# Kernel optimization log

Hardware: AMD Instinct MI355X
Metric: run time of the kernel (lower is better)

The kernel has to match this reference:

```python
import jax, jax.numpy as jnp
import numpy as np

N = 50000
E = 800000
D_IN, D_HID, D_OUT = 128, 128, 64


def _glorot(key, shape):
    fan_in, fan_out = shape[1], shape[0]
    lim = np.sqrt(6.0 / (fan_in + fan_out))
    return jax.random.uniform(key, shape, jnp.float32, -lim, lim)


def setup_inputs() -> dict:
    key = jax.random.key(0)
    ks = jax.random.split(key, 12)
    x = jax.random.normal(ks[0], (N, D_IN), jnp.float32)
    edge_index = jax.random.randint(ks[1], (2, E), 0, N, jnp.int32)
    edge_attr = jax.random.uniform(ks[2], (E,), jnp.float32)
    return {
        "x": x,
        "edge_index": edge_index,
        "edge_attr": edge_attr,
        # conv1: in -> hidden
        "W1_rel": _glorot(ks[3], (D_HID, D_IN)),
        "b1_rel": jnp.zeros((D_HID,), jnp.float32),
        "W1_root": _glorot(ks[4], (D_HID, D_IN)),
        # conv_mu: hidden -> out
        "Wmu_rel": _glorot(ks[5], (D_OUT, D_HID)),
        "bmu_rel": jnp.zeros((D_OUT,), jnp.float32),
        "Wmu_root": _glorot(ks[6], (D_OUT, D_HID)),
        # conv_logvar: hidden -> out
        "Wlv_rel": _glorot(ks[7], (D_OUT, D_HID)),
        "blv_rel": jnp.zeros((D_OUT,), jnp.float32),
        "Wlv_root": _glorot(ks[8], (D_OUT, D_HID)),
    }


def sage_conv(x, src, dst, ew, W_rel, b_rel, W_root, n_nodes):
    # message: edge_weight * x_j  (gather from source nodes)
    msg = x[src] * ew[:, None]                                   # [E, d]
    agg = jax.ops.segment_sum(msg, dst, num_segments=n_nodes)    # [N, d]
    cnt = jax.ops.segment_sum(jnp.ones_like(ew), dst, num_segments=n_nodes)
    mean = agg / jnp.maximum(cnt, 1.0)[:, None]                  # scatter-mean
    return mean @ W_rel.T + b_rel + x @ W_root.T


def reference(x, edge_index, edge_attr, W1_rel, b1_rel, W1_root,
              Wmu_rel, bmu_rel, Wmu_root, Wlv_rel, blv_rel, Wlv_root):
    src, dst = edge_index[0], edge_index[1]
    h = jax.nn.elu(sage_conv(x, src, dst, edge_attr, W1_rel, b1_rel, W1_root, N))
    mu = sage_conv(h, src, dst, edge_attr, Wmu_rel, bmu_rel, Wmu_root, N)
    logvar = sage_conv(h, src, dst, edge_attr, Wlv_rel, blv_rel, Wlv_root, N)
    return mu, logvar
```

## Files before the change

### kernel.cpp

```cpp
#include <hip/hip_runtime.h>
#include <hip/hip_bf16.h>
#include <math.h>

#define NNODES 50000
#define NEDGES 800000
#define NRANGE 6250
#define NC     64
#define CHUNK_E (NEDGES / NC)
#define NSLICE 4
#define SLICE_E (CHUNK_E / NSLICE)

using short8 = __attribute__((ext_vector_type(8))) short;
using f32x4  = __attribute__((ext_vector_type(4))) float;
typedef unsigned long long u64;

__device__ __forceinline__ short f2bf(float f) {
    __hip_bfloat16 h = __float2bfloat16(f);
    return *reinterpret_cast<short*>(&h);
}


__global__ __launch_bounds__(256)
void prep_kernel(const float* __restrict__ x, __hip_bfloat16* __restrict__ xb,
                 const float* __restrict__ w0, const float* __restrict__ w1,
                 const float* __restrict__ w2, const float* __restrict__ w3,
                 const float* __restrict__ w4, const float* __restrict__ w5,
                 __hip_bfloat16* __restrict__ Wb) {
    int b = blockIdx.x;
    int tid = threadIdx.x;
    if (b < 3125) {
        int i = b * 256 + tid;
        const float4* p = (const float4*)x + (size_t)i * 2;
        float4 a = p[0], c = p[1];
        short8 o;
        o[0] = f2bf(a.x); o[1] = f2bf(a.y); o[2] = f2bf(a.z); o[3] = f2bf(a.w);
        o[4] = f2bf(c.x); o[5] = f2bf(c.y); o[6] = f2bf(c.z); o[7] = f2bf(c.w);
        *reinterpret_cast<short8*>((short*)xb + (size_t)i * 8) = o;
    } else {
        int i = (b - 3125) * 256 + tid;
        const float* src; int off;
        if      (i < 16384) { src = w0; off = 0; }
        else if (i < 32768) { src = w1; off = 16384; }
        else if (i < 40960) { src = w2; off = 32768; }
        else if (i < 49152) { src = w3; off = 40960; }
        else if (i < 57344) { src = w4; off = 49152; }
        else                { src = w5; off = 57344; }
        Wb[i] = __float2bfloat16(src[i - off]);
    }
}


__global__ __launch_bounds__(256)
void hist_kernel(const int* __restrict__ dst, unsigned int* __restrict__ partial,
                 unsigned char* __restrict__ rank8) {
    __shared__ unsigned int hist[NNODES / 4];
    int c = blockIdx.x;
    int tid = threadIdx.x;
    for (int i = tid; i < NNODES / 4; i += 256) hist[i] = 0;
    __syncthreads();
    int base = c * CHUNK_E;
    for (int e = base + tid; e < base + CHUNK_E; e += 256) {
        int d = dst[e];
        int sh = 8 * (d & 3);
        unsigned int old = atomicAdd(&hist[d >> 2], 1u << sh);
        rank8[e] = (unsigned char)((old >> sh) & 0xffu);
    }
    __syncthreads();
    unsigned int* outp = partial + (size_t)c * (NNODES / 4);
    for (int i = tid; i < NNODES / 4; i += 256) outp[i] = hist[i];
}


__global__ __launch_bounds__(1024)
void scan1_kernel(const unsigned int* __restrict__ partial,
                  unsigned char* __restrict__ cbase,
                  int* __restrict__ excl, int* __restrict__ bsum) {
    __shared__ int sdata[1024];
    int tid = threadIdx.x;
    int n = blockIdx.x * 1024 + tid;
    int deg = 0;
    if (n < NNODES) {
        int sh = 8 * (n & 3);
        int idx = n >> 2;
        unsigned int packed = 0;
        unsigned int* cbout = (unsigned int*)(cbase + (size_t)n * NC);
#pragma unroll 4
        for (int c = 0; c < NC; ++c) {
            unsigned int w = partial[(size_t)c * (NNODES / 4) + idx];
            unsigned int cc = (w >> sh) & 0xffu;
            packed |= ((unsigned int)(deg & 0xff)) << (8 * (c & 3));
            deg += (int)cc;
            if ((c & 3) == 3) { cbout[c >> 2] = packed; packed = 0; }
        }
    }
    sdata[tid] = deg;
    __syncthreads();
    for (int off = 1; off < 1024; off <<= 1) {
        int t = (tid >= off) ? sdata[tid - off] : 0;
        __syncthreads();
        sdata[tid] += t;
        __syncthreads();
    }
    if (n < NNODES) excl[n] = sdata[tid] - deg;
    if (tid == 1023) bsum[blockIdx.x] = sdata[1023];
}

__global__ __launch_bounds__(64)
void scan2_kernel(int* __restrict__ bsum, int nb) {
    int lane = threadIdx.x;
    int v = (lane < nb) ? bsum[lane] : 0;
    int incl = v;
    for (int off = 1; off < 64; off <<= 1) {
        int t = __shfl_up(incl, off);
        if (lane >= off) incl += t;
    }
    if (lane < nb) bsum[lane] = incl - v;
    if (lane == 63) bsum[nb] = incl;
}


__global__ __launch_bounds__(256)
void fill_kernel(const int* __restrict__ src, const int* __restrict__ dst,
                 const float* __restrict__ ew,
                 const int* __restrict__ excl, const int* __restrict__ bsum,
                 const unsigned char* __restrict__ cbase,
                 const unsigned char* __restrict__ rank8,
                 u64* __restrict__ edges) {
    int b = blockIdx.x;
    int r = b & 7;
    int t = b >> 3;
    int c = t & (NC - 1);
    int s = t >> 6;
    int lo = r * NRANGE;
    int base = c * CHUNK_E + s * SLICE_E;
    int end = base + SLICE_E;
    for (int e = base + threadIdx.x; e < end; e += 256) {
        int d = dst[e];
        unsigned int dl = (unsigned int)(d - lo);
        if (dl < NRANGE) {
            int slot = excl[d] + bsum[d >> 10] + (int)cbase[(size_t)d * NC + c] + (int)rank8[e];
            u64 pack = ((u64)(unsigned int)__float_as_int(ew[e]) << 32) | (unsigned int)src[e];
            edges[slot] = pack;
        }
    }
}


__device__ __forceinline__ void gstep(u64 e, const unsigned int* __restrict__ Fb,
                                      int lane, float& ax, float& ay) {
    unsigned int v = Fb[(size_t)(unsigned int)e * 64 + lane];
    float w = __uint_as_float((unsigned int)(e >> 32));
    ax += __uint_as_float(v << 16) * w;
    ay += __uint_as_float(v & 0xffff0000u) * w;
}

__global__ __launch_bounds__(256)
void gather_mean_kernel(const unsigned int* __restrict__ Fb,
                        const int* __restrict__ excl, const int* __restrict__ bsum,
                        const u64* __restrict__ edges,
                        unsigned int* __restrict__ outb,
                        int n_nodes, int E) {
    int node = (blockIdx.x * blockDim.x + threadIdx.x) >> 6;
    int lane = threadIdx.x & 63;
    if (node >= n_nodes) return;
    int beg = excl[node] + bsum[node >> 10];
    int end = (node + 1 < n_nodes) ? (excl[node + 1] + bsum[(node + 1) >> 10]) : E;
    beg = __builtin_amdgcn_readfirstlane(beg);
    end = __builtin_amdgcn_readfirstlane(end);

    float ax[8], ay[8];
#pragma unroll
    for (int j = 0; j < 8; ++j) { ax[j] = 0.f; ay[j] = 0.f; }

    int s = beg;
    for (; s + 8 <= end; s += 8) {
        u64 e[8];
#pragma unroll
        for (int j = 0; j < 8; ++j) e[j] = __builtin_nontemporal_load(edges + s + j);
#pragma unroll
        for (int j = 0; j < 8; ++j) gstep(e[j], Fb, lane, ax[j], ay[j]);
    }
    if (s + 4 <= end) {
        u64 e[4];
#pragma unroll
        for (int j = 0; j < 4; ++j) e[j] = __builtin_nontemporal_load(edges + s + j);
#pragma unroll
        for (int j = 0; j < 4; ++j) gstep(e[j], Fb, lane, ax[j], ay[j]);
        s += 4;
    }
    if (s + 2 <= end) {
        u64 e0 = __builtin_nontemporal_load(edges + s);
        u64 e1 = __builtin_nontemporal_load(edges + s + 1);
        gstep(e0, Fb, lane, ax[0], ay[0]);
        gstep(e1, Fb, lane, ax[1], ay[1]);
        s += 2;
    }
    if (s < end) {
        u64 e0 = __builtin_nontemporal_load(edges + s);
        gstep(e0, Fb, lane, ax[0], ay[0]);
    }
#pragma unroll
    for (int j = 4; j < 8; ++j) { ax[j - 4] += ax[j]; ay[j - 4] += ay[j]; }
    float axs = (ax[0] + ax[1]) + (ax[2] + ax[3]);
    float ays = (ay[0] + ay[1]) + (ay[2] + ay[3]);
    float inv = 1.f / fmaxf((float)(end - beg), 1.f);
    unsigned int lo = (unsigned int)(unsigned short)f2bf(axs * inv);
    unsigned int hi = (unsigned int)(unsigned short)f2bf(ays * inv);
    outb[(size_t)node * 64 + lane] = lo | (hi << 16);
}


__global__ __launch_bounds__(256)
void linear1_mfma(const __hip_bfloat16* __restrict__ Ab1,
                  const __hip_bfloat16* __restrict__ Ab2,
                  const __hip_bfloat16* __restrict__ Wb,
                  const float* __restrict__ bias,
                  __hip_bfloat16* __restrict__ outb,
                  int n_nodes) {
    int wid  = threadIdx.x >> 6;
    int lane = threadIdx.x & 63;
    int nodeBase = blockIdx.x * 64 + wid * 16;
    int m  = lane & 15;
    int kq = lane >> 4;
    int node = nodeBase + m;
    int nodeC = (node < n_nodes) ? node : (n_nodes - 1);

    short8 a1[4], a2[4];
    const short* A1p = (const short*)Ab1 + (size_t)nodeC * 128 + kq * 8;
    const short* A2p = (const short*)Ab2 + (size_t)nodeC * 128 + kq * 8;
#pragma unroll
    for (int kk = 0; kk < 4; ++kk) {
        a1[kk] = *(const short8*)(A1p + kk * 32);
        a2[kk] = *(const short8*)(A2p + kk * 32);
    }
    const short* Wrel  = (const short*)Wb;
    const short* Wroot = (const short*)Wb + 16384;

#pragma unroll
    for (int c = 0; c < 8; ++c) {
        f32x4 acc = {0.f, 0.f, 0.f, 0.f};
        const short* b1p = Wrel  + (size_t)(c * 16 + m) * 128 + kq * 8;
        const short* b2p = Wroot + (size_t)(c * 16 + m) * 128 + kq * 8;
#pragma unroll
        for (int kk = 0; kk < 4; ++kk) {
            short8 bw1 = *(const short8*)(b1p + kk * 32);
            acc = __builtin_amdgcn_mfma_f32_16x16x32_bf16(a1[kk], bw1, acc, 0, 0, 0);
            short8 bw2 = *(const short8*)(b2p + kk * 32);
            acc = __builtin_amdgcn_mfma_f32_16x16x32_bf16(a2[kk], bw2, acc, 0, 0, 0);
        }
        int col = c * 16 + m;
        float b = bias[col];
#pragma unroll
        for (int i = 0; i < 4; ++i) {
            int gn = nodeBase + kq * 4 + i;
            if (gn < n_nodes) {
                float v = acc[i] + b;
                v = (v > 0.f) ? v : expm1f(v);
                outb[(size_t)gn * 128 + col] = __float2bfloat16(v);
            }
        }
    }
}

__global__ __launch_bounds__(256)
void linear2_mfma(const __hip_bfloat16* __restrict__ Ab1,
                  const __hip_bfloat16* __restrict__ Ab2,
                  const __hip_bfloat16* __restrict__ Wb,
                  const float* __restrict__ bmu, const float* __restrict__ blv,
                  float* __restrict__ out,
                  int n_nodes) {
    int wid  = threadIdx.x >> 6;
    int lane = threadIdx.x & 63;
    int nodeBase = blockIdx.x * 64 + wid * 16;
    int m  = lane & 15;
    int kq = lane >> 4;
    int node = nodeBase + m;
    int nodeC = (node < n_nodes) ? node : (n_nodes - 1);

    short8 a1[4], a2[4];
    const short* A1p = (const short*)Ab1 + (size_t)nodeC * 128 + kq * 8;
    const short* A2p = (const short*)Ab2 + (size_t)nodeC * 128 + kq * 8;
#pragma unroll
    for (int kk = 0; kk < 4; ++kk) {
        a1[kk] = *(const short8*)(A1p + kk * 32);
        a2[kk] = *(const short8*)(A2p + kk * 32);
    }
    const short* WmuR = (const short*)Wb + 32768;
    const short* WmuT = (const short*)Wb + 40960;
    const short* WlvR = (const short*)Wb + 49152;
    const short* WlvT = (const short*)Wb + 57344;

#pragma unroll
    for (int c = 0; c < 4; ++c) {
        f32x4 accMu = {0.f, 0.f, 0.f, 0.f};
        f32x4 accLv = {0.f, 0.f, 0.f, 0.f};
        size_t wrow = (size_t)(c * 16 + m) * 128 + kq * 8;
#pragma unroll
        for (int kk = 0; kk < 4; ++kk) {
            short8 bm1 = *(const short8*)(WmuR + wrow + kk * 32);
            accMu = __builtin_amdgcn_mfma_f32_16x16x32_bf16(a1[kk], bm1, accMu, 0, 0, 0);
            short8 bm2 = *(const short8*)(WmuT + wrow + kk * 32);
            accMu = __builtin_amdgcn_mfma_f32_16x16x32_bf16(a2[kk], bm2, accMu, 0, 0, 0);
            short8 bl1 = *(const short8*)(WlvR + wrow + kk * 32);
            accLv = __builtin_amdgcn_mfma_f32_16x16x32_bf16(a1[kk], bl1, accLv, 0, 0, 0);
            short8 bl2 = *(const short8*)(WlvT + wrow + kk * 32);
            accLv = __builtin_amdgcn_mfma_f32_16x16x32_bf16(a2[kk], bl2, accLv, 0, 0, 0);
        }
        int col = c * 16 + m;
        float bm = bmu[col], bl = blv[col];
#pragma unroll
        for (int i = 0; i < 4; ++i) {
            int gn = nodeBase + kq * 4 + i;
            if (gn < n_nodes) {
                out[(size_t)gn * 64 + col] = accMu[i] + bm;
                out[(size_t)NNODES * 64 + (size_t)gn * 64 + col] = accLv[i] + bl;
            }
        }
    }
}

extern "C" void kernel_launch(void* const* d_in, const int* in_sizes, int n_in,
                              void* d_out, int out_size, void* d_ws, size_t ws_size,
                              hipStream_t stream) {
    const float* x        = (const float*)d_in[0];
    const int*   eidx     = (const int*)d_in[1];
    const float* eattr    = (const float*)d_in[2];
    const float* W1_rel   = (const float*)d_in[3];
    const float* b1_rel   = (const float*)d_in[4];
    const float* W1_root  = (const float*)d_in[5];
    const float* Wmu_rel  = (const float*)d_in[6];
    const float* bmu_rel  = (const float*)d_in[7];
    const float* Wmu_root = (const float*)d_in[8];
    const float* Wlv_rel  = (const float*)d_in[9];
    const float* blv_rel  = (const float*)d_in[10];
    const float* Wlv_root = (const float*)d_in[11];
    float* out = (float*)d_out;

    const int N = NNODES, E = NEDGES;
    const int nb = (N + 1023) / 1024;
    const int* src = eidx;
    const int* dst = eidx + E;

    char* ws = (char*)d_ws;
    size_t off = 0;
    int* excl = (int*)(ws + off); off += (size_t)N * 4;
    int* bsum = (int*)(ws + off); off += 256;
    off = (off + 63) & ~(size_t)63;
    unsigned int* partial = (unsigned int*)(ws + off); off += (size_t)NC * (N / 4) * 4;
    unsigned char* cbase  = (unsigned char*)(ws + off); off += (size_t)N * NC;
    unsigned char* rank8  = (unsigned char*)(ws + off); off += (size_t)E;
    off = (off + 63) & ~(size_t)63;
    u64* edges = (u64*)(ws + off); off += (size_t)E * 8;
    __hip_bfloat16* xb    = (__hip_bfloat16*)(ws + off); off += (size_t)N * 128 * 2;
    __hip_bfloat16* meanb = (__hip_bfloat16*)(ws + off); off += (size_t)N * 128 * 2;
    __hip_bfloat16* hb    = (__hip_bfloat16*)(ws + off); off += (size_t)N * 128 * 2;
    __hip_bfloat16* Wb    = (__hip_bfloat16*)(ws + off); off += 65536 * 2;

    prep_kernel<<<3381, 256, 0, stream>>>(x, xb, W1_rel, W1_root, Wmu_rel, Wmu_root,
                                          Wlv_rel, Wlv_root, Wb);
    hist_kernel<<<NC, 256, 0, stream>>>(dst, partial, rank8);
    scan1_kernel<<<nb, 1024, 0, stream>>>(partial, cbase, excl, bsum);
    scan2_kernel<<<1, 64, 0, stream>>>(bsum, nb);
    fill_kernel<<<NC * 8 * NSLICE, 256, 0, stream>>>(src, dst, eattr, excl, bsum,
                                                     cbase, rank8, edges);

    gather_mean_kernel<<<(N * 64 + 255) / 256, 256, 0, stream>>>(
        (const unsigned int*)xb, excl, bsum, edges, (unsigned int*)meanb, N, E);
    linear1_mfma<<<(N + 63) / 64, 256, 0, stream>>>(meanb, xb, Wb, b1_rel, hb, N);
    gather_mean_kernel<<<(N * 64 + 255) / 256, 256, 0, stream>>>(
        (const unsigned int*)hb, excl, bsum, edges, (unsigned int*)meanb, N, E);
    linear2_mfma<<<(N + 63) / 64, 256, 0, stream>>>(meanb, hb, Wb, bmu_rel, blv_rel, out, N);
}
```

Measured before the change: 213.4 us.

## Slice feature matrices into column blocks for cache-local gathers; fuse histogram into prep

Stores the bf16 node features (x, mean, h) as four column slices of 32 features each, so each slice of the whole table (about 3.2 MB) is more likely to stay in cache during the random gather. The gather kernel now uses 16 lanes per node per slice, and blocks are interleaved across slice and node half so concurrent blocks hit the same slice. The linear kernels read and write through the sliced layout. The histogram kernel is merged into the prep launch to drop one launch. In exchange, the edge list is read four times per layer, and each 16-lane group has its own loop bound, so nodes with different degrees make those groups diverge within a wavefront.

```diff
diff --git a/kernel.cpp b/kernel.cpp
--- a/kernel.cpp
+++ b/kernel.cpp
@@ -9,6 +9,10 @@
 #define CHUNK_E (NEDGES / NC)
 #define NSLICE 4
 #define SLICE_E (CHUNK_E / NSLICE)
+#define NHALF (NNODES / 2)
+
+#define SLICE_STRIDE_U (NNODES * 16)
+#define SLICE_STRIDE_S (NNODES * 32)
 
 using short8 = __attribute__((ext_vector_type(8))) short;
 using f32x4  = __attribute__((ext_vector_type(4))) float;
@@ -25,19 +29,38 @@
                  const float* __restrict__ w0, const float* __restrict__ w1,
                  const float* __restrict__ w2, const float* __restrict__ w3,
                  const float* __restrict__ w4, const float* __restrict__ w5,
-                 __hip_bfloat16* __restrict__ Wb) {
+                 __hip_bfloat16* __restrict__ Wb,
+                 const int* __restrict__ dst, unsigned int* __restrict__ partial,
+                 unsigned char* __restrict__ rank8) {
+    __shared__ unsigned int hist[NNODES / 4];
     int b = blockIdx.x;
     int tid = threadIdx.x;
-    if (b < 3125) {
-        int i = b * 256 + tid;
-        const float4* p = (const float4*)x + (size_t)i * 2;
-        float4 a = p[0], c = p[1];
+    if (b < 64) {
+        int c = b;
+        for (int i = tid; i < NNODES / 4; i += 256) hist[i] = 0;
+        __syncthreads();
+        int base = c * CHUNK_E;
+        for (int e = base + tid; e < base + CHUNK_E; e += 256) {
+            int d = dst[e];
+            int sh = 8 * (d & 3);
+            unsigned int old = atomicAdd(&hist[d >> 2], 1u << sh);
+            rank8[e] = (unsigned char)((old >> sh) & 0xffu);
+        }
+        __syncthreads();
+        unsigned int* outp = partial + (size_t)c * (NNODES / 4);
+        for (int i = tid; i < NNODES / 4; i += 256) outp[i] = hist[i];
+    } else if (b < 3189) {
+        int i = (b - 64) * 256 + tid;
+        int node = i >> 4, t = i & 15;
+        const float4* p = (const float4*)(x + (size_t)node * 128 + t * 8);
+        float4 a = p[0], c4 = p[1];
         short8 o;
         o[0] = f2bf(a.x); o[1] = f2bf(a.y); o[2] = f2bf(a.z); o[3] = f2bf(a.w);
-        o[4] = f2bf(c.x); o[5] = f2bf(c.y); o[6] = f2bf(c.z); o[7] = f2bf(c.w);
-        *reinterpret_cast<short8*>((short*)xb + (size_t)i * 8) = o;
+        o[4] = f2bf(c4.x); o[5] = f2bf(c4.y); o[6] = f2bf(c4.z); o[7] = f2bf(c4.w);
+        short* dstp = (short*)xb + (size_t)(t >> 2) * SLICE_STRIDE_S + (size_t)node * 32 + (t & 3) * 8;
+        *reinterpret_cast<short8*>(dstp) = o;
     } else {
-        int i = (b - 3125) * 256 + tid;
+        int i = (b - 3189) * 256 + tid;
         const float* src; int off;
         if      (i < 16384) { src = w0; off = 0; }
         else if (i < 32768) { src = w1; off = 16384; }
@@ -47,27 +70,6 @@
         else                { src = w5; off = 57344; }
         Wb[i] = __float2bfloat16(src[i - off]);
     }
-}
-
-
-__global__ __launch_bounds__(256)
-void hist_kernel(const int* __restrict__ dst, unsigned int* __restrict__ partial,
-                 unsigned char* __restrict__ rank8) {
-    __shared__ unsigned int hist[NNODES / 4];
-    int c = blockIdx.x;
-    int tid = threadIdx.x;
-    for (int i = tid; i < NNODES / 4; i += 256) hist[i] = 0;
-    __syncthreads();
-    int base = c * CHUNK_E;
-    for (int e = base + tid; e < base + CHUNK_E; e += 256) {
-        int d = dst[e];
-        int sh = 8 * (d & 3);
-        unsigned int old = atomicAdd(&hist[d >> 2], 1u << sh);
-        rank8[e] = (unsigned char)((old >> sh) & 0xffu);
-    }
-    __syncthreads();
-    unsigned int* outp = partial + (size_t)c * (NNODES / 4);
-    for (int i = tid; i < NNODES / 4; i += 256) outp[i] = hist[i];
 }
 
 
@@ -146,9 +148,9 @@
 }
 
 
-__device__ __forceinline__ void gstep(u64 e, const unsigned int* __restrict__ Fb,
-                                      int lane, float& ax, float& ay) {
-    unsigned int v = Fb[(size_t)(unsigned int)e * 64 + lane];
+__device__ __forceinline__ void gstep16(u64 e, const unsigned int* __restrict__ F,
+                                        float& ax, float& ay) {
+    unsigned int v = F[(size_t)(unsigned int)e * 16];
     float w = __uint_as_float((unsigned int)(e >> 32));
     ax += __uint_as_float(v << 16) * w;
     ay += __uint_as_float(v & 0xffff0000u) * w;
@@ -159,54 +161,44 @@
                         const int* __restrict__ excl, const int* __restrict__ bsum,
                         const u64* __restrict__ edges,
                         unsigned int* __restrict__ outb,
-                        int n_nodes, int E) {
-    int node = (blockIdx.x * blockDim.x + threadIdx.x) >> 6;
-    int lane = threadIdx.x & 63;
-    if (node >= n_nodes) return;
+                        int E) {
+    int b = blockIdx.x;
+    int r = b & 7;
+    int slice = r & 3;
+    int half = r >> 2;
+    int nb = b >> 3;
+    int g = threadIdx.x >> 4;
+    int lane16 = threadIdx.x & 15;
+    int nlocal = nb * 16 + g;
+    if (nlocal >= NHALF) return;
+    int node = half * NHALF + nlocal;
     int beg = excl[node] + bsum[node >> 10];
-    int end = (node + 1 < n_nodes) ? (excl[node + 1] + bsum[(node + 1) >> 10]) : E;
-    beg = __builtin_amdgcn_readfirstlane(beg);
-    end = __builtin_amdgcn_readfirstlane(end);
-
-    float ax[8], ay[8];
-#pragma unroll
-    for (int j = 0; j < 8; ++j) { ax[j] = 0.f; ay[j] = 0.f; }
-
+    int end = (node + 1 < NNODES) ? (excl[node + 1] + bsum[(node + 1) >> 10]) : E;
+    const unsigned int* F = Fb + (size_t)slice * SLICE_STRIDE_U + lane16;
+
+    float ax0 = 0.f, ay0 = 0.f, ax1 = 0.f, ay1 = 0.f;
+    float ax2 = 0.f, ay2 = 0.f, ax3 = 0.f, ay3 = 0.f;
     int s = beg;
-    for (; s + 8 <= end; s += 8) {
-        u64 e[8];
-#pragma unroll
-        for (int j = 0; j < 8; ++j) e[j] = __builtin_nontemporal_load(edges + s + j);
-#pragma unroll
-        for (int j = 0; j < 8; ++j) gstep(e[j], Fb, lane, ax[j], ay[j]);
-    }
-    if (s + 4 <= end) {
-        u64 e[4];
-#pragma unroll
-        for (int j = 0; j < 4; ++j) e[j] = __builtin_nontemporal_load(edges + s + j);
-#pragma unroll
-        for (int j = 0; j < 4; ++j) gstep(e[j], Fb, lane, ax[j], ay[j]);
-        s += 4;
-    }
-    if (s + 2 <= end) {
+    for (; s + 4 <= end; s += 4) {
+        u64 e0 = __builtin_nontemporal_load(edges + s + 0);
+        u64 e1 = __builtin_nontemporal_load(edges + s + 1);
+        u64 e2 = __builtin_nontemporal_load(edges + s + 2);
+        u64 e3 = __builtin_nontemporal_load(edges + s + 3);
+        gstep16(e0, F, ax0, ay0);
+        gstep16(e1, F, ax1, ay1);
+        gstep16(e2, F, ax2, ay2);
+        gstep16(e3, F, ax3, ay3);
+    }
+    for (; s < end; ++s) {
         u64 e0 = __builtin_nontemporal_load(edges + s);
-        u64 e1 = __builtin_nontemporal_load(edges + s + 1);
-        gstep(e0, Fb, lane, ax[0], ay[0]);
-        gstep(e1, Fb, lane, ax[1], ay[1]);
-        s += 2;
-    }
-    if (s < end) {
-        u64 e0 = __builtin_nontemporal_load(edges + s);
-        gstep(e0, Fb, lane, ax[0], ay[0]);
-    }
-#pragma unroll
-    for (int j = 4; j < 8; ++j) { ax[j - 4] += ax[j]; ay[j - 4] += ay[j]; }
-    float axs = (ax[0] + ax[1]) + (ax[2] + ax[3]);
-    float ays = (ay[0] + ay[1]) + (ay[2] + ay[3]);
+        gstep16(e0, F, ax0, ay0);
+    }
+    float axs = (ax0 + ax1) + (ax2 + ax3);
+    float ays = (ay0 + ay1) + (ay2 + ay3);
     float inv = 1.f / fmaxf((float)(end - beg), 1.f);
     unsigned int lo = (unsigned int)(unsigned short)f2bf(axs * inv);
     unsigned int hi = (unsigned int)(unsigned short)f2bf(ays * inv);
-    outb[(size_t)node * 64 + lane] = lo | (hi << 16);
+    outb[(size_t)slice * SLICE_STRIDE_U + (size_t)node * 16 + lane16] = lo | (hi << 16);
 }
 
 
@@ -226,12 +218,12 @@
     int nodeC = (node < n_nodes) ? node : (n_nodes - 1);
 
     short8 a1[4], a2[4];
-    const short* A1p = (const short*)Ab1 + (size_t)nodeC * 128 + kq * 8;
-    const short* A2p = (const short*)Ab2 + (size_t)nodeC * 128 + kq * 8;
+    const short* A1p = (const short*)Ab1 + (size_t)nodeC * 32 + kq * 8;
+    const short* A2p = (const short*)Ab2 + (size_t)nodeC * 32 + kq * 8;
 #pragma unroll
     for (int kk = 0; kk < 4; ++kk) {
-        a1[kk] = *(const short8*)(A1p + kk * 32);
-        a2[kk] = *(const short8*)(A2p + kk * 32);
+        a1[kk] = *(const short8*)(A1p + (size_t)kk * SLICE_STRIDE_S);
+        a2[kk] = *(const short8*)(A2p + (size_t)kk * SLICE_STRIDE_S);
     }
     const short* Wrel  = (const short*)Wb;
     const short* Wroot = (const short*)Wb + 16384;
@@ -250,13 +242,14 @@
         }
         int col = c * 16 + m;
         float b = bias[col];
+        short* op = (short*)outb + (size_t)(c >> 1) * SLICE_STRIDE_S + (c & 1) * 16 + m;
 #pragma unroll
         for (int i = 0; i < 4; ++i) {
             int gn = nodeBase + kq * 4 + i;
             if (gn < n_nodes) {
                 float v = acc[i] + b;
                 v = (v > 0.f) ? v : expm1f(v);
-                outb[(size_t)gn * 128 + col] = __float2bfloat16(v);
+                op[(size_t)gn * 32] = f2bf(v);
             }
         }
     }
@@ -278,12 +271,12 @@
     int nodeC = (node < n_nodes) ? node : (n_nodes - 1);
 
     short8 a1[4], a2[4];
-    const short* A1p = (const short*)Ab1 + (size_t)nodeC * 128 + kq * 8;
-    const short* A2p = (const short*)Ab2 + (size_t)nodeC * 128 + kq * 8;
+    const short* A1p = (const short*)Ab1 + (size_t)nodeC * 32 + kq * 8;
+    const short* A2p = (const short*)Ab2 + (size_t)nodeC * 32 + kq * 8;
 #pragma unroll
     for (int kk = 0; kk < 4; ++kk) {
-        a1[kk] = *(const short8*)(A1p + kk * 32);
-        a2[kk] = *(const short8*)(A2p + kk * 32);
+        a1[kk] = *(const short8*)(A1p + (size_t)kk * SLICE_STRIDE_S);
+        a2[kk] = *(const short8*)(A2p + (size_t)kk * SLICE_STRIDE_S);
     }
     const short* WmuR = (const short*)Wb + 32768;
     const short* WmuT = (const short*)Wb + 40960;
@@ -356,18 +349,18 @@
     __hip_bfloat16* hb    = (__hip_bfloat16*)(ws + off); off += (size_t)N * 128 * 2;
     __hip_bfloat16* Wb    = (__hip_bfloat16*)(ws + off); off += 65536 * 2;
 
-    prep_kernel<<<3381, 256, 0, stream>>>(x, xb, W1_rel, W1_root, Wmu_rel, Wmu_root,
-                                          Wlv_rel, Wlv_root, Wb);
-    hist_kernel<<<NC, 256, 0, stream>>>(dst, partial, rank8);
+    prep_kernel<<<3445, 256, 0, stream>>>(x, xb, W1_rel, W1_root, Wmu_rel, Wmu_root,
+                                          Wlv_rel, Wlv_root, Wb, dst, partial, rank8);
     scan1_kernel<<<nb, 1024, 0, stream>>>(partial, cbase, excl, bsum);
     scan2_kernel<<<1, 64, 0, stream>>>(bsum, nb);
     fill_kernel<<<NC * 8 * NSLICE, 256, 0, stream>>>(src, dst, eattr, excl, bsum,
                                                      cbase, rank8, edges);
 
-    gather_mean_kernel<<<(N * 64 + 255) / 256, 256, 0, stream>>>(
-        (const unsigned int*)xb, excl, bsum, edges, (unsigned int*)meanb, N, E);
+    const int gblocks = ((NHALF + 15) / 16) * 8;
+    gather_mean_kernel<<<gblocks, 256, 0, stream>>>(
+        (const unsigned int*)xb, excl, bsum, edges, (unsigned int*)meanb, E);
     linear1_mfma<<<(N + 63) / 64, 256, 0, stream>>>(meanb, xb, Wb, b1_rel, hb, N);
-    gather_mean_kernel<<<(N * 64 + 255) / 256, 256, 0, stream>>>(
-        (const unsigned int*)hb, excl, bsum, edges, (unsigned int*)meanb, N, E);
+    gather_mean_kernel<<<gblocks, 256, 0, stream>>>(
+        (const unsigned int*)hb, excl, bsum, edges, (unsigned int*)meanb, E);
     linear2_mfma<<<(N + 63) / 64, 256, 0, stream>>>(meanb, hb, Wb, bmu_rel, blv_rel, out, N);
 }
```

Result: slower. 255.5 us (+19.7%).
